# Optimization experiments

Measured on AMD Instinct MI355X. Metric: run time of the kernel, lower is better.

The kernel has to match this reference:

```python
import jax, jax.numpy as jnp
import numpy as np

NODE_TYPES = ["patient", "visit", "symptom", "procedure", "disease", "drug"]
N = {"patient": 20000, "visit": 100000, "symptom": 4000, "procedure": 8000,
     "disease": 10000, "drug": 4000}
D = 128          # embedding_dim == hidden_channels
N_LAYERS = 4     # conv1..conv4
# (src, dst) per relation; reverse edges included so every node type gets messages
REL = [("patient", "visit"), ("visit", "patient"),
       ("visit", "symptom"), ("symptom", "visit"),
       ("visit", "procedure"), ("procedure", "visit"),
       ("visit", "disease"), ("disease", "visit"),
       ("visit", "drug"), ("drug", "visit")]
E_FWD = {("patient", "visit"): 100000, ("visit", "symptom"): 300000,
         ("visit", "procedure"): 200000, ("visit", "disease"): 250000,
         ("visit", "drug"): 300000}
EI_NAMES = ["ei_pv", "ei_vp", "ei_vs", "ei_sv", "ei_vpr", "ei_prv",
            "ei_vd", "ei_dv", "ei_vdr", "ei_drv"]
E_LABEL = 200000


def setup_inputs() -> dict:
    key = jax.random.key(0)
    ks = iter(jax.random.split(key, 64))
    inp = {}
    for nt in NODE_TYPES:
        inp[f"node_id_{nt}"] = jnp.arange(N[nt], dtype=jnp.int32)
        inp[f"emb_{nt}"] = jax.random.normal(next(ks), (N[nt], D), jnp.float32)
    for name, (src, dst) in zip(EI_NAMES, REL):
        e = E_FWD.get((src, dst), E_FWD.get((dst, src)))
        row = jax.random.randint(next(ks), (e,), 0, N[src], dtype=jnp.int32)
        col = jax.random.randint(next(ks), (e,), 0, N[dst], dtype=jnp.int32)
        inp[name] = jnp.stack([row, col])
    R = len(REL)
    inp["W_l"] = jax.random.normal(next(ks), (N_LAYERS, R, D, D), jnp.float32) * 0.05
    inp["b_l"] = jnp.zeros((N_LAYERS, R, D), jnp.float32)
    inp["W_r"] = jax.random.normal(next(ks), (N_LAYERS, R, D, D), jnp.float32) * 0.05
    inp["cls_w1"] = jax.random.normal(next(ks), (2 * D, D), jnp.float32) * 0.05
    inp["cls_b1"] = jnp.zeros((D,), jnp.float32)
    inp["cls_w2"] = jax.random.normal(next(ks), (D, 1), jnp.float32) * 0.05
    inp["cls_b2"] = jnp.zeros((1,), jnp.float32)
    row = jax.random.randint(next(ks), (E_LABEL,), 0, N["visit"], dtype=jnp.int32)
    col = jax.random.randint(next(ks), (E_LABEL,), 0, N["drug"], dtype=jnp.int32)
    inp["edge_label_index"] = jnp.stack([row, col])
    inp["edge_label"] = jax.random.bernoulli(next(ks), 0.5, (E_LABEL,)).astype(jnp.float32)
    return inp


def _hetero_sage_layer(x, eis, Wl, bl, Wr):
    # to_hetero semantics: out[dst] = sum over edge types (src,rel,dst) of
    #   SAGEConv_rel: lin_l(mean_j x[src][j]) + lin_r(x[dst])   (PyG defaults)
    out = {nt: jnp.zeros_like(v) for nt, v in x.items()}
    for r, (src, dst) in enumerate(REL):
        ei = eis[r]
        n_dst = x[dst].shape[0]
        msg = jax.ops.segment_sum(x[src][ei[0]], ei[1], num_segments=n_dst)
        deg = jax.ops.segment_sum(jnp.ones((ei.shape[1],), x[src].dtype), ei[1],
                                  num_segments=n_dst)
        mean = msg / jnp.maximum(deg, 1.0)[:, None]  # empty segments stay 0 as in PyG
        out[dst] = out[dst] + mean @ Wl[r] + bl[r] + x[dst] @ Wr[r]
    return out


def reference(node_id_patient, node_id_visit, node_id_symptom, node_id_procedure,
              node_id_disease, node_id_drug,
              emb_patient, emb_visit, emb_symptom, emb_procedure, emb_disease, emb_drug,
              ei_pv, ei_vp, ei_vs, ei_sv, ei_vpr, ei_prv, ei_vd, ei_dv, ei_vdr, ei_drv,
              W_l, b_l, W_r, cls_w1, cls_b1, cls_w2, cls_b2,
              edge_label_index, edge_label):
    x = {"patient": emb_patient[node_id_patient],
         "visit": emb_visit[node_id_visit],
         "symptom": emb_symptom[node_id_symptom],
         "procedure": emb_procedure[node_id_procedure],
         "disease": emb_disease[node_id_disease],
         "drug": emb_drug[node_id_drug]}
    eis = [ei_pv, ei_vp, ei_vs, ei_sv, ei_vpr, ei_prv, ei_vd, ei_dv, ei_vdr, ei_drv]
    for l in range(N_LAYERS):
        x = _hetero_sage_layer(x, eis, W_l[l], b_l[l], W_r[l])
        if l < N_LAYERS - 1:  # relu after conv1..conv3 only; dropout is eval-mode identity
            x = {k: jax.nn.relu(v) for k, v in x.items()}
    # Classifier: gather visit/drug node features per labeled edge, concat, MLP
    zv = x["visit"][edge_label_index[0]]
    zd = x["drug"][edge_label_index[1]]
    h = jax.nn.relu(jnp.concatenate([zv, zd], axis=-1) @ cls_w1 + cls_b1)
    pred = (h @ cls_w2 + cls_b2).reshape(-1)
    # BCE with logits: softplus(z) - z*y, mean-reduced
    loss = jnp.mean(jax.nn.softplus(pred) - pred * edge_label)
    return loss, pred
```

## Files before the change

### kernel.cpp

```cpp
#include <hip/hip_runtime.h>
#include <cmath>


typedef _Float16 f16x8 __attribute__((ext_vector_type(8)));
typedef float f32x4 __attribute__((ext_vector_type(4)));

#define NREL 10
#define NCOUNTS 546000
#define NEDGES  2300000
#define NVISIT  100000
#define NVEDGES 1150000
#define PLW 546816
#define WT_ELEMS (4 * PLW + 69632)
#define XELEMS 18688000UL
#define SELEMS 5888000UL
#define NBKT 873
#define BCAP 5056
#define NMERGE 391
#define CONV_BLKS 9125

struct BkMeta {
  const int* ei[NREL]; int E[NREL]; int cbc[NREL]; int ndst[NREL];
  int sh[NREL]; int bb[NREL]; int nb[NREL];
};
struct PreMeta {
  const float* emb[6]; const int* nid[6]; int off[6];
  const float* W_l; const float* b_l; const float* W_r; const float* cw1;
  _Float16* Wt; float* visitSumB;
};
struct MTask {
  const _Float16* AH0; const _Float16* AL0;
  const _Float16* AH1; const _Float16* AL1;
  const _Float16* W;
  const float* bias;
  _Float16* outH; _Float16* outL;
  int M, blkOff, K, relu;
};
struct MMeta { MTask t[6]; int nTasks; };
struct F1Meta {
  const int* rp[5]; _Float16* mH[5]; _Float16* mL[5]; int aM[5]; int aOff[5];
  int nAgg; int aggTotal;
  const _Float16* gAH[5]; const _Float16* gAL[5]; const _Float16* gW[5];
  _Float16* gY[5]; int gM[5]; int gOff[5]; int nG;
};

__device__ __forceinline__ void conv0_body(const PreMeta& pm, int bc, int tid,
                                           _Float16* __restrict__ H,
                                           _Float16* __restrict__ L) {
  int i = bc * 256 + tid;
  if (i >= 146000 * 16) return;
  int g = i >> 4, q = i & 15;
  int t = 0;
  #pragma unroll
  for (int k = 1; k < 6; ++k) if (g >= pm.off[k]) t = k;
  int row = g - pm.off[t];
  int s = pm.nid[t][row];
  const float* p = pm.emb[t] + (size_t)s * 128 + q * 8;
  float4 v0 = *(const float4*)p;
  float4 v1 = *(const float4*)(p + 4);
  float v[8] = {v0.x, v0.y, v0.z, v0.w, v1.x, v1.y, v1.z, v1.w};
  f16x8 h, l;
  #pragma unroll
  for (int j = 0; j < 8; ++j) {
    h[j] = (_Float16)v[j];
    l[j] = (_Float16)(v[j] - (float)h[j]);
  }
  size_t o = (size_t)g * 128 + q * 8;
  *(f16x8*)(H + o) = h;
  *(f16x8*)(L + o) = l;
}

__device__ __forceinline__ void prep_body(const PreMeta& pm, int gid) {
  const int visitRel[5] = {0, 3, 5, 7, 9};
  const int inRel[5] = {1, 2, 4, 6, 8};
  if (gid < 1048576) {
    int l = gid >> 18, o = gid & 262143;
    float val; size_t wbase; int n, k, Kpad;
    if (o < 163840) {
      int t = o >> 15, e = o & 32767;
      k = e >> 7; n = e & 127; Kpad = 264;
      int r = inRel[t];
      val = (k < 128) ? pm.W_l[(size_t)(l * 10 + r) * 16384 + k * 128 + n]
                      : pm.W_r[(size_t)(l * 10 + r) * 16384 + (k - 128) * 128 + n];
      wbase = (size_t)l * PLW + t * 67584;
    } else if (o < 245760) {
      int q = (o - 163840) >> 14, e = (o - 163840) & 16383;
      k = e >> 7; n = e & 127; Kpad = 136;
      val = pm.W_l[(size_t)(l * 10 + visitRel[q]) * 16384 + k * 128 + n];
      wbase = (size_t)l * PLW + 337920 + q * 34816;
    } else {
      int e = o - 245760;
      k = e >> 7; n = e & 127; Kpad = 136;
      val = 0.f;
      #pragma unroll
      for (int q = 0; q < 5; ++q)
        val += pm.W_r[(size_t)(l * 10 + visitRel[q]) * 16384 + k * 128 + n];
      wbase = (size_t)l * PLW + 512000;
    }
    _Float16 h = (_Float16)val;
    _Float16 lo = (_Float16)(val - (float)h);
    pm.Wt[wbase + (size_t)n * Kpad + k] = h;
    pm.Wt[wbase + (size_t)(128 + n) * Kpad + k] = lo;
  } else if (gid < 1081344) {
    int e = gid - 1048576;
    int k = e >> 7, n = e & 127;
    float val = pm.cw1[(size_t)k * 128 + n];
    _Float16 h = (_Float16)val;
    _Float16 lo = (_Float16)(val - (float)h);
    size_t wbase = (size_t)4 * PLW + (k < 128 ? 0 : 34816);
    int kk = k & 127;
    pm.Wt[wbase + (size_t)n * 136 + kk] = h;
    pm.Wt[wbase + (size_t)(128 + n) * 136 + kk] = lo;
  } else if (gid < 1081856) {
    int e = gid - 1081344;
    int l = e >> 7, c = e & 127;
    float val = 0.f;
    #pragma unroll
    for (int q = 0; q < 5; ++q) val += pm.b_l[(l * 10 + visitRel[q]) * 128 + c];
    pm.visitSumB[e] = val;
  }
}

__global__ __launch_bounds__(256) void k1_p1_prep(BkMeta bm, PreMeta pm,
                                                  int* __restrict__ bcur,
                                                  int* __restrict__ bdata) {
  __shared__ int cnt[128];
  __shared__ int base[128];
  __shared__ unsigned short rnk[4096];
  int b = blockIdx.x;
  int tid = threadIdx.x;
  if (b >= 740) {
    prep_body(pm, (b - 740) * 256 + tid);
    return;
  }
  int r = b / 74;
  int bx = b - r * 74;
  int E = bm.E[r], sh = bm.sh[r], bb = bm.bb[r], nb = bm.nb[r];
  if (tid < 128) cnt[tid] = 0;
  __syncthreads();
  int e0 = bx * 4096;
  if (e0 >= E) return;
  const int* dstp = bm.ei[r] + E;
  const int* srcp = bm.ei[r];
  #pragma unroll
  for (int i = 0; i < 16; ++i) {
    int e = e0 + i * 256 + tid;
    if (e < E) {
      int bk = dstp[e] >> sh;
      rnk[i * 256 + tid] = (unsigned short)atomicAdd(&cnt[bk], 1);
    }
  }
  __syncthreads();
  if (tid < nb && cnt[tid] > 0) base[tid] = atomicAdd(&bcur[bb + tid], cnt[tid]);
  __syncthreads();
  #pragma unroll
  for (int i = 0; i < 16; ++i) {
    int e = e0 + i * 256 + tid;
    if (e < E) {
      int d = dstp[e];
      int bk = d >> sh;
      int pos = base[bk] + (int)rnk[i * 256 + tid];
      if (pos < BCAP)
        bdata[(size_t)(bb + bk) * BCAP + pos] = ((d & ((1 << sh) - 1)) << 17) | srcp[e];
    }
  }
}

__global__ __launch_bounds__(256) void k2_p2a_conv(BkMeta bm, PreMeta pm,
                                                   const int* __restrict__ bcur,
                                                   const int* __restrict__ bdata,
                                                   int* __restrict__ counts,
                                                   _Float16* __restrict__ H,
                                                   _Float16* __restrict__ L,
                                                   int convBase) {
  __shared__ int hist[2048];
  int b = blockIdx.x;
  int tid = threadIdx.x;
  if (b >= NBKT) {
    conv0_body(pm, convBase + b - NBKT, tid, H, L);
    return;
  }
  int g = b;
  int r = 0;
  #pragma unroll
  for (int i = 1; i < NREL; ++i) if (g >= bm.bb[i]) r = i;
  int lb = g - bm.bb[r];
  int sh = bm.sh[r], dpb = 1 << sh;
  for (int d = tid; d < dpb; d += 256) hist[d] = 0;
  __syncthreads();
  int cnt = bcur[g]; if (cnt > BCAP) cnt = BCAP;
  const int* bd = bdata + (size_t)g * BCAP;
  for (int i = tid; i < cnt; i += 256) atomicAdd(&hist[((unsigned)bd[i]) >> 17], 1);
  __syncthreads();
  int dBase = lb << sh;
  int dMax = bm.ndst[r] - dBase; if (dMax > dpb) dMax = dpb;
  for (int d = tid; d < dMax; d += 256) counts[bm.cbc[r] + dBase + d] = hist[d];
}

__global__ __launch_bounds__(1024) void scan1(const int* __restrict__ counts,
                                              int* __restrict__ partials) {
  __shared__ int s[1024];
  int i = blockIdx.x * 1024 + threadIdx.x;
  s[threadIdx.x] = (i < NCOUNTS) ? counts[i] : 0;
  __syncthreads();
  for (int off = 512; off > 0; off >>= 1) {
    if (threadIdx.x < off) s[threadIdx.x] += s[threadIdx.x + off];
    __syncthreads();
  }
  if (threadIdx.x == 0) partials[blockIdx.x] = s[0];
}

__global__ __launch_bounds__(1024) void scan2(int* __restrict__ partials, int nb) {
  __shared__ int s[1024];
  int t = threadIdx.x;
  int v = (t < nb) ? partials[t] : 0;
  s[t] = v;
  __syncthreads();
  for (int off = 1; off < 1024; off <<= 1) {
    int add = (t >= off) ? s[t - off] : 0;
    __syncthreads();
    s[t] += add;
    __syncthreads();
  }
  if (t < nb) partials[t] = s[t] - v;
}

__global__ __launch_bounds__(1024) void scan3(const int* __restrict__ counts,
                                              int* __restrict__ prefix,
                                              const int* __restrict__ partials) {
  __shared__ int s[1024];
  int t = threadIdx.x;
  int i = blockIdx.x * 1024 + t;
  int v = (i < NCOUNTS) ? counts[i] : 0;
  s[t] = v;
  __syncthreads();
  for (int off = 1; off < 1024; off <<= 1) {
    int add = (t >= off) ? s[t - off] : 0;
    __syncthreads();
    s[t] += add;
    __syncthreads();
  }
  int P = partials[blockIdx.x] + s[t] - v;
  if (i < NCOUNTS) prefix[i] = P;
  if (blockIdx.x == 0 && t == 0) prefix[NCOUNTS] = NEDGES;
}

__global__ __launch_bounds__(256) void k3_p2b_conv(BkMeta bm, PreMeta pm,
                                                   const int* __restrict__ bcur,
                                                   const int* __restrict__ bdata,
                                                   const int* __restrict__ prefix,
                                                   int* __restrict__ esrc,
                                                   _Float16* __restrict__ H,
                                                   _Float16* __restrict__ L,
                                                   int convBase) {
  __shared__ int pk[BCAP];
  __shared__ int srt[BCAP];
  __shared__ int cur[2048];
  __shared__ int part[256];
  __shared__ int baseSh;
  int b = blockIdx.x;
  int tid = threadIdx.x;
  if (b >= NBKT) {
    conv0_body(pm, convBase + b - NBKT, tid, H, L);
    return;
  }
  int g = b;
  int r = 0;
  #pragma unroll
  for (int i = 1; i < NREL; ++i) if (g >= bm.bb[i]) r = i;
  int lb = g - bm.bb[r];
  int sh = bm.sh[r], dpb = 1 << sh;
  int cnt = bcur[g]; if (cnt > BCAP) cnt = BCAP;
  const int* bd = bdata + (size_t)g * BCAP;
  for (int d = tid; d < dpb; d += 256) cur[d] = 0;
  for (int i = tid; i < cnt; i += 256) pk[i] = bd[i];
  __syncthreads();
  for (int i = tid; i < cnt; i += 256) atomicAdd(&cur[((unsigned)pk[i]) >> 17], 1);
  __syncthreads();
  int seg = (dpb + 255) >> 8;
  int s = 0;
  int b0 = tid * seg;
  for (int j = 0; j < seg; ++j) {
    int idx = b0 + j;
    if (idx < dpb) { int v = cur[idx]; cur[idx] = s; s += v; }
  }
  part[tid] = s;
  __syncthreads();
  for (int off = 1; off < 256; off <<= 1) {
    int add = (tid >= off) ? part[tid - off] : 0;
    __syncthreads();
    part[tid] += add;
    __syncthreads();
  }
  int myoff = part[tid] - s;
  for (int j = 0; j < seg; ++j) {
    int idx = b0 + j;
    if (idx < dpb) cur[idx] += myoff;
  }
  if (tid == 0) baseSh = prefix[bm.cbc[r] + (lb << sh)];
  __syncthreads();
  for (int i = tid; i < cnt; i += 256) {
    int p = pk[i];
    int pos = atomicAdd(&cur[((unsigned)p) >> 17], 1);
    srt[pos] = p & 0x1FFFF;
  }
  __syncthreads();
  int base = baseSh;
  for (int i = tid; i < cnt; i += 256) esrc[base + i] = srt[i];
}

__global__ __launch_bounds__(256) void k4_merge_conv(PreMeta pm,
                                                     const int* __restrict__ prefix,
                                                     const int* __restrict__ esrc,
                                                     int* __restrict__ mprefix,
                                                     int2* __restrict__ mesrc,
                                                     _Float16* __restrict__ H,
                                                     _Float16* __restrict__ L,
                                                     int convBase) {
  int b = blockIdx.x;
  int tid = threadIdx.x;
  if (b >= NMERGE) {
    conv0_body(pm, convBase + b - NMERGE, tid, H, L);
    return;
  }
  const int cbc[5]  = {0, 124000, 232000, 342000, 446000};
  const int yoff[5] = {0, 20000, 24000, 32000, 42000};
  int v = b * 256 + tid;
  if (v >= NVISIT) return;
  int e0[5], e1[5];
  int base = 0;
  #pragma unroll
  for (int q = 0; q < 5; ++q) {
    e0[q] = prefix[cbc[q] + v];
    e1[q] = prefix[cbc[q] + v + 1];
    base += e0[q] - prefix[cbc[q]];
  }
  mprefix[v] = base;
  if (v == NVISIT - 1) {
    int t = base;
    #pragma unroll
    for (int q = 0; q < 5; ++q) t += e1[q] - e0[q];
    mprefix[NVISIT] = t;
  }
  int pos = base;
  #pragma unroll
  for (int q = 0; q < 5; ++q) {
    int d = e1[q] - e0[q];
    if (d > 0) {
      int wb = __float_as_int(1.f / (float)d);
      for (int e = e0[q]; e < e1[q]; ++e)
        mesrc[pos++] = make_int2(yoff[q] + esrc[e], wb);
    }
  }
}

__global__ __launch_bounds__(256, 8) void fused1(F1Meta f,
                                                 const _Float16* __restrict__ xvH,
                                                 const int* __restrict__ esrc) {
  int b = blockIdx.x;
  int tid = threadIdx.x;
  if (b < f.aggTotal) {
    int t = 0;
    #pragma unroll
    for (int i = 1; i < 5; ++i) if (i < f.nAgg && b >= f.aOff[i]) t = i;
    int row = (b - f.aOff[t]) * 16 + (tid >> 4);
    if (row >= f.aM[t]) return;
    int q = tid & 15;
    const int* rp = f.rp[t];
    int e0 = rp[row], e1 = rp[row + 1];
    float a[8];
    #pragma unroll
    for (int j = 0; j < 8; ++j) a[j] = 0.f;
    int e = e0;
    for (; e + 4 <= e1; e += 4) {
      int s0 = esrc[e], s1 = esrc[e + 1], s2 = esrc[e + 2], s3 = esrc[e + 3];
      f16x8 v0 = *(const f16x8*)(xvH + (size_t)s0 * 128 + q * 8);
      f16x8 v1 = *(const f16x8*)(xvH + (size_t)s1 * 128 + q * 8);
      f16x8 v2 = *(const f16x8*)(xvH + (size_t)s2 * 128 + q * 8);
      f16x8 v3 = *(const f16x8*)(xvH + (size_t)s3 * 128 + q * 8);
      #pragma unroll
      for (int j = 0; j < 8; ++j)
        a[j] += ((float)v0[j] + (float)v1[j]) + ((float)v2[j] + (float)v3[j]);
    }
    for (; e < e1; ++e) {
      int s = esrc[e];
      f16x8 v = *(const f16x8*)(xvH + (size_t)s * 128 + q * 8);
      #pragma unroll
      for (int j = 0; j < 8; ++j) a[j] += (float)v[j];
    }
    float inv = (e1 > e0) ? 1.f / (float)(e1 - e0) : 0.f;
    f16x8 h, l;
    #pragma unroll
    for (int j = 0; j < 8; ++j) {
      float v = a[j] * inv;
      h[j] = (_Float16)v;
      l[j] = (_Float16)(v - (float)h[j]);
    }
    size_t o = (size_t)row * 128 + q * 8;
    *(f16x8*)(f.mH[t] + o) = h;
    *(f16x8*)(f.mL[t] + o) = l;
    return;
  }
  b -= f.aggTotal;
  int g = 0;
  #pragma unroll
  for (int i = 1; i < 5; ++i) if (i < f.nG && b >= f.gOff[i]) g = i;
  int blockRow = (b - f.gOff[g]) * 32;
  int lane = tid & 63, wave = tid >> 6;
  int quad = lane >> 4, lm = lane & 15;
  int wr = wave >> 1, wc = wave & 1;
  const _Float16* AH = f.gAH[g];
  const _Float16* AL = f.gAL[g];
  const _Float16* W = f.gW[g];
  int M = f.gM[g];
  int ar = blockRow + wr * 16 + lm;
  if (ar >= M) ar = M - 1;
  f32x4 acc[4];
  #pragma unroll
  for (int nt = 0; nt < 4; ++nt) acc[nt] = (f32x4){0.f, 0.f, 0.f, 0.f};
  for (int ks = 0; ks < 128; ks += 32) {
    f16x8 ah = *(const f16x8*)(AH + (size_t)ar * 128 + ks + quad * 8);
    f16x8 al = *(const f16x8*)(AL + (size_t)ar * 128 + ks + quad * 8);
    #pragma unroll
    for (int nt = 0; nt < 4; ++nt) {
      int n = wc * 64 + nt * 16 + lm;
      f16x8 bh = *(const f16x8*)(W + (size_t)n * 136 + ks + quad * 8);
      f16x8 bl = *(const f16x8*)(W + (size_t)(128 + n) * 136 + ks + quad * 8);
      acc[nt] = __builtin_amdgcn_mfma_f32_16x16x32_f16(ah, bh, acc[nt], 0, 0, 0);
      acc[nt] = __builtin_amdgcn_mfma_f32_16x16x32_f16(ah, bl, acc[nt], 0, 0, 0);
      acc[nt] = __builtin_amdgcn_mfma_f32_16x16x32_f16(al, bh, acc[nt], 0, 0, 0);
    }
  }
  _Float16* Y = f.gY[g];
  #pragma unroll
  for (int i = 0; i < 4; ++i) {
    int grow = blockRow + wr * 16 + quad * 4 + i;
    if (grow >= M) continue;
    #pragma unroll
    for (int nt = 0; nt < 4; ++nt)
      Y[(size_t)grow * 128 + wc * 64 + nt * 16 + lm] = (_Float16)acc[nt][i];
  }
}

__global__ __launch_bounds__(256) void agg_visit(const int* __restrict__ mprefix,
                                                 const int2* __restrict__ mesrc,
                                                 const _Float16* __restrict__ YH,
                                                 _Float16* __restrict__ xvH,
                                                 _Float16* __restrict__ xvL, int doRelu) {
  int row = blockIdx.x * 16 + (threadIdx.x >> 4);
  if (row >= NVISIT) return;
  int q = threadIdx.x & 15;
  size_t o = (size_t)row * 128 + q * 8;
  f16x8 h0 = *(f16x8*)(xvH + o);
  f16x8 l0 = *(f16x8*)(xvL + o);
  float a[8];
  #pragma unroll
  for (int j = 0; j < 8; ++j) a[j] = (float)h0[j] + (float)l0[j];
  int e0 = mprefix[row], e1 = mprefix[row + 1];
  int e = e0;
  for (; e + 4 <= e1; e += 4) {
    int2 p0 = mesrc[e], p1 = mesrc[e + 1], p2 = mesrc[e + 2], p3 = mesrc[e + 3];
    f16x8 v0 = *(const f16x8*)(YH + (size_t)p0.x * 128 + q * 8);
    f16x8 v1 = *(const f16x8*)(YH + (size_t)p1.x * 128 + q * 8);
    f16x8 v2 = *(const f16x8*)(YH + (size_t)p2.x * 128 + q * 8);
    f16x8 v3 = *(const f16x8*)(YH + (size_t)p3.x * 128 + q * 8);
    float w0 = __int_as_float(p0.y), w1 = __int_as_float(p1.y);
    float w2 = __int_as_float(p2.y), w3 = __int_as_float(p3.y);
    #pragma unroll
    for (int j = 0; j < 8; ++j)
      a[j] += (w0 * (float)v0[j] + w1 * (float)v1[j]) +
              (w2 * (float)v2[j] + w3 * (float)v3[j]);
  }
  for (; e < e1; ++e) {
    int2 p = mesrc[e];
    f16x8 v = *(const f16x8*)(YH + (size_t)p.x * 128 + q * 8);
    float w = __int_as_float(p.y);
    #pragma unroll
    for (int j = 0; j < 8; ++j) a[j] += w * (float)v[j];
  }
  f16x8 h, l;
  #pragma unroll
  for (int j = 0; j < 8; ++j) {
    float v = doRelu ? fmaxf(a[j], 0.f) : a[j];
    h[j] = (_Float16)v;
    l[j] = (_Float16)(v - (float)h[j]);
  }
  *(f16x8*)(xvH + o) = h;
  *(f16x8*)(xvL + o) = l;
}

__global__ __launch_bounds__(256, 2) void mgemm(MMeta mm) {
  int b = blockIdx.x;
  int ti = 0;
  for (int i = 1; i < mm.nTasks; ++i) if (b >= mm.t[i].blkOff) ti = i;
  MTask tk = mm.t[ti];
  int blockRow = (b - tk.blkOff) * 128;
  int Kpad = tk.K + 8;

  __shared__ _Float16 Ash[2][128][72];
  int tid = threadIdx.x;
  int wave = tid >> 6, lane = tid & 63;
  int quad = lane >> 4, lm = lane & 15;
  int wr = wave >> 1, wc = wave & 1;

  f32x4 acc[4][4];
  #pragma unroll
  for (int i = 0; i < 4; ++i)
    #pragma unroll
    for (int j = 0; j < 4; ++j) acc[i][j] = (f32x4){0.f, 0.f, 0.f, 0.f};

  const _Float16* wrowH[4];
  const _Float16* wrowL[4];
  #pragma unroll
  for (int nt = 0; nt < 4; ++nt) {
    int n = wc * 64 + nt * 16 + lm;
    wrowH[nt] = tk.W + (size_t)n * Kpad;
    wrowL[nt] = tk.W + (size_t)(128 + n) * Kpad;
  }

  int sr = tid >> 1, sk = (tid & 1) * 32;
  int gr = blockRow + sr; if (gr >= tk.M) gr = tk.M - 1;
  for (int k0 = 0; k0 < tk.K; k0 += 64) {
    const _Float16* AH = (k0 < 128) ? tk.AH0 : tk.AH1;
    const _Float16* AL = (k0 < 128) ? tk.AL0 : tk.AL1;
    size_t abase = (size_t)gr * 128 + (k0 & 127) + sk;
    #pragma unroll
    for (int c = 0; c < 4; ++c) {
      *(f16x8*)&Ash[0][sr][sk + c * 8] = *(const f16x8*)(AH + abase + c * 8);
      *(f16x8*)&Ash[1][sr][sk + c * 8] = *(const f16x8*)(AL + abase + c * 8);
    }
    __syncthreads();
    #pragma unroll
    for (int ks = 0; ks < 64; ks += 32) {
      int kf = k0 + ks + quad * 8;
      f16x8 bh[4], bl[4];
      #pragma unroll
      for (int nt = 0; nt < 4; ++nt) {
        bh[nt] = *(const f16x8*)(wrowH[nt] + kf);
        bl[nt] = *(const f16x8*)(wrowL[nt] + kf);
      }
      #pragma unroll
      for (int mt = 0; mt < 4; ++mt) {
        int r = wr * 64 + mt * 16 + lm;
        f16x8 ah = *(const f16x8*)&Ash[0][r][ks + quad * 8];
        f16x8 al = *(const f16x8*)&Ash[1][r][ks + quad * 8];
        #pragma unroll
        for (int nt = 0; nt < 4; ++nt) {
          acc[mt][nt] = __builtin_amdgcn_mfma_f32_16x16x32_f16(ah, bh[nt], acc[mt][nt], 0, 0, 0);
          acc[mt][nt] = __builtin_amdgcn_mfma_f32_16x16x32_f16(ah, bl[nt], acc[mt][nt], 0, 0, 0);
          acc[mt][nt] = __builtin_amdgcn_mfma_f32_16x16x32_f16(al, bh[nt], acc[mt][nt], 0, 0, 0);
        }
      }
    }
    __syncthreads();
  }

  float bv[4];
  #pragma unroll
  for (int nt = 0; nt < 4; ++nt)
    bv[nt] = tk.bias ? tk.bias[wc * 64 + nt * 16 + lm] : 0.f;
  #pragma unroll
  for (int mt = 0; mt < 4; ++mt) {
    #pragma unroll
    for (int i = 0; i < 4; ++i) {
      int grow = blockRow + wr * 64 + mt * 16 + quad * 4 + i;
      if (grow >= tk.M) continue;
      size_t ob = (size_t)grow * 128 + wc * 64 + lm;
      #pragma unroll
      for (int nt = 0; nt < 4; ++nt) {
        float v = acc[mt][nt][i] + bv[nt];
        if (tk.relu) v = fmaxf(v, 0.f);
        _Float16 h = (_Float16)v;
        tk.outH[ob + nt * 16] = h;
        if (tk.outL) tk.outL[ob + nt * 16] = (_Float16)(v - (float)h);
      }
    }
  }
}

__global__ __launch_bounds__(256) void cls_edge(
    const _Float16* __restrict__ UH, const _Float16* __restrict__ UL,
    const _Float16* __restrict__ VH, const _Float16* __restrict__ VL,
    const int* __restrict__ eli, const float* __restrict__ w2,
    const float* __restrict__ b2, const float* __restrict__ y,
    float* __restrict__ lossOut, float* __restrict__ pred, int M) {
  __shared__ float lsum[4];
  int tid = threadIdx.x;
  int q = tid & 15;
  int lane = tid & 63;
  float w2v[8];
  #pragma unroll
  for (int j = 0; j < 8; ++j) w2v[j] = w2[q * 8 + j];
  float bias = b2[0];
  float lacc = 0.f;
  int e0 = blockIdx.x * 128 + (tid >> 4);
  #pragma unroll
  for (int p = 0; p < 8; ++p) {
    int e = e0 + p * 16;
    if (e < M) {
      int vi = eli[e], di = eli[M + e];
      size_t uo = (size_t)vi * 128 + q * 8;
      size_t vo = (size_t)di * 128 + q * 8;
      f16x8 uh = *(const f16x8*)(UH + uo);
      f16x8 ul = *(const f16x8*)(UL + uo);
      f16x8 vh = *(const f16x8*)(VH + vo);
      f16x8 vl = *(const f16x8*)(VL + vo);
      float part = 0.f;
      #pragma unroll
      for (int j = 0; j < 8; ++j) {
        float t = ((float)uh[j] + (float)ul[j]) + ((float)vh[j] + (float)vl[j]);
        part += fmaxf(t, 0.f) * w2v[j];
      }
      part += __shfl_xor(part, 1);
      part += __shfl_xor(part, 2);
      part += __shfl_xor(part, 4);
      part += __shfl_xor(part, 8);
      if (q == 0) {
        float z = part + bias;
        pred[e] = z;
        lacc += fmaxf(z, 0.f) + log1pf(expf(-fabsf(z))) - z * y[e];
      }
    }
  }
  lacc += __shfl_xor(lacc, 16);
  lacc += __shfl_xor(lacc, 32);
  if (lane == 0) lsum[tid >> 6] = lacc;
  __syncthreads();
  if (tid == 0)
    atomicAdd(lossOut, (lsum[0] + lsum[1] + lsum[2] + lsum[3]) * (1.0f / 200000.0f));
}

extern "C" void kernel_launch(void* const* d_in, const int* in_sizes, int n_in,
                              void* d_out, int out_size, void* d_ws, size_t ws_size,
                              hipStream_t stream) {
  static const int kRows[6] = {20000, 100000, 4000, 8000, 10000, 4000};
  static const int kOff[6]  = {0, 20000, 120000, 124000, 132000, 142000};
  static const int kSmallT[5]   = {0, 2, 3, 4, 5};
  static const int kInRel[5]    = {1, 2, 4, 6, 8};
  static const int kCbcIn[5]    = {100000, 120000, 224000, 332000, 442000};
  static const int kYOff[5]     = {0, 20000, 24000, 32000, 42000};
  static const int kBOff[5]     = {0, 157, 189, 252, 331};
  static const int kAggOff[5]   = {0, 1250, 1500, 2000, 2625};
  static const int kLeanOff[5]  = {0, 625, 750, 1000, 1313};
  const int kAggTotal = 2875, kLeanTotal = 1438;
  const int kConvK2 = 3000, kConvK3 = 1500, kConvK4 = CONV_BLKS - 4500;
  static const int kCbcA[NREL]  = {0, 100000, 120000, 124000, 224000,
                                   232000, 332000, 342000, 442000, 446000};
  static const int kEhA[NREL]   = {100000, 100000, 300000, 300000, 200000,
                                   200000, 250000, 250000, 300000, 300000};
  static const int kNdst[NREL]  = {100000, 20000, 4000, 100000, 8000,
                                   100000, 10000, 100000, 4000, 100000};
  static const int kSh[NREL]    = {11, 9, 5, 10, 7, 10, 7, 10, 5, 10};
  static const int kNB[NREL]    = {49, 40, 125, 98, 63, 98, 79, 98, 125, 98};
  static const int kBB[NREL]    = {0, 49, 89, 214, 312, 375, 473, 552, 650, 775};

  const float* W_l = (const float*)d_in[22];
  const float* b_l = (const float*)d_in[23];
  const float* W_r = (const float*)d_in[24];
  const float* cw1 = (const float*)d_in[25];
  const float* cb1 = (const float*)d_in[26];
  const float* cw2 = (const float*)d_in[27];
  const float* cb2 = (const float*)d_in[28];
  const int* eli = (const int*)d_in[29];
  const float* ylab = (const float*)d_in[30];

  _Float16* H = (_Float16*)d_ws;
  _Float16* L = H + XELEMS;
  _Float16* meanH = L + XELEMS;
  _Float16* meanL = meanH + SELEMS;
  _Float16* YH = meanL + SELEMS;
  _Float16* Wt = YH + SELEMS;
  int* prefix = (int*)(Wt + WT_ELEMS);
  int* counts = prefix + 546004;
  int* esrc = counts + NCOUNTS;
  int* partials = esrc + NEDGES;
  float* visitSumB = (float*)(partials + 1024);
  int* bcur = (int*)(visitSumB + 512);
  int* bdata = bcur + 1024;

  int* mprefix = counts;
  int2* mesrc = (int2*)bdata;

  _Float16* UH = meanH;
  _Float16* VH = meanH + (size_t)NVISIT * 128;
  _Float16* VL = VH + (size_t)4000 * 128;
  _Float16* UL = (_Float16*)prefix;

  BkMeta bm;
  for (int r = 0; r < NREL; ++r) {
    bm.ei[r] = (const int*)d_in[12 + r];
    bm.E[r] = kEhA[r];
    bm.cbc[r] = kCbcA[r];
    bm.ndst[r] = kNdst[r];
    bm.sh[r] = kSh[r];
    bm.bb[r] = kBB[r];
    bm.nb[r] = kNB[r];
  }

  PreMeta pm;
  for (int t = 0; t < 6; ++t) {
    pm.nid[t] = (const int*)d_in[2 * t];
    pm.emb[t] = (const float*)d_in[2 * t + 1];
    pm.off[t] = kOff[t];
  }
  pm.W_l = W_l; pm.b_l = b_l; pm.W_r = W_r; pm.cw1 = cw1;
  pm.Wt = Wt; pm.visitSumB = visitSumB;

  hipMemsetAsync(bcur, 0, NBKT * sizeof(int), stream);
  hipMemsetAsync(d_out, 0, sizeof(float), stream);

  k1_p1_prep<<<dim3(740 + 4226), 256, 0, stream>>>(bm, pm, bcur, bdata);
  k2_p2a_conv<<<dim3(NBKT + kConvK2), 256, 0, stream>>>(bm, pm, bcur, bdata,
                                                        counts, H, L, 0);
  scan1<<<534, 1024, 0, stream>>>(counts, partials);
  scan2<<<1, 1024, 0, stream>>>(partials, 534);
  scan3<<<534, 1024, 0, stream>>>(counts, prefix, partials);
  k3_p2b_conv<<<dim3(NBKT + kConvK3), 256, 0, stream>>>(bm, pm, bcur, bdata,
                                                        prefix, esrc, H, L, kConvK2);
  k4_merge_conv<<<dim3(NMERGE + kConvK4), 256, 0, stream>>>(pm, prefix, esrc,
                                                            mprefix, mesrc, H, L,
                                                            kConvK2 + kConvK3);

  _Float16* xvH = H + (size_t)kOff[1] * 128;
  _Float16* xvL = L + (size_t)kOff[1] * 128;

  for (int l = 0; l < 4; ++l) {
    int doRelu = (l < 3);
    int last = (l == 3);
    _Float16* LW = Wt + (size_t)l * PLW;

    F1Meta f1;
    if (!last) {
      for (int t = 0; t < 5; ++t) {
        f1.rp[t] = prefix + kCbcIn[t];
        f1.mH[t] = meanH + (size_t)kYOff[t] * 128;
        f1.mL[t] = meanL + (size_t)kYOff[t] * 128;
        f1.aM[t] = kRows[kSmallT[t]];
        f1.aOff[t] = kAggOff[t];
      }
      f1.nAgg = 5;
      f1.aggTotal = kAggTotal;
    } else {
      f1.rp[0] = prefix + kCbcIn[4];
      f1.mH[0] = meanH + (size_t)kYOff[4] * 128;
      f1.mL[0] = meanL + (size_t)kYOff[4] * 128;
      f1.aM[0] = 4000;
      f1.aOff[0] = 0;
      for (int t = 1; t < 5; ++t) { f1.rp[t] = nullptr; f1.mH[t] = nullptr; f1.mL[t] = nullptr; f1.aM[t] = 0; f1.aOff[t] = 0; }
      f1.nAgg = 1;
      f1.aggTotal = 250;
    }
    for (int q = 0; q < 5; ++q) {
      size_t so = (size_t)kOff[kSmallT[q]] * 128;
      f1.gAH[q] = H + so;
      f1.gAL[q] = L + so;
      f1.gW[q] = LW + 337920 + (size_t)q * 34816;
      f1.gY[q] = YH + (size_t)kYOff[q] * 128;
      f1.gM[q] = kRows[kSmallT[q]];
      f1.gOff[q] = kLeanOff[q];
    }
    f1.nG = 5;
    fused1<<<dim3(f1.aggTotal + kLeanTotal), 256, 0, stream>>>(f1, xvH, esrc);

    MMeta m;
    if (!last) {
      m.nTasks = 6;
      for (int t = 0; t < 5; ++t) {
        size_t mo = (size_t)kYOff[t] * 128;
        size_t so = (size_t)kOff[kSmallT[t]] * 128;
        m.t[t].AH0 = meanH + mo; m.t[t].AL0 = meanL + mo;
        m.t[t].AH1 = H + so;     m.t[t].AL1 = L + so;
        m.t[t].W = LW + (size_t)t * 67584;
        m.t[t].bias = b_l + (size_t)(l * 10 + kInRel[t]) * 128;
        m.t[t].outH = H + so;    m.t[t].outL = L + so;
        m.t[t].M = kRows[kSmallT[t]];
        m.t[t].blkOff = kBOff[t];
        m.t[t].K = 256;
        m.t[t].relu = doRelu;
      }
      m.t[5].AH0 = xvH; m.t[5].AL0 = xvL;
      m.t[5].AH1 = nullptr; m.t[5].AL1 = nullptr;
      m.t[5].W = LW + 512000;
      m.t[5].bias = visitSumB + l * 128;
      m.t[5].outH = xvH; m.t[5].outL = xvL;
      m.t[5].M = NVISIT;
      m.t[5].blkOff = 363;
      m.t[5].K = 128;
      m.t[5].relu = 0;
      mgemm<<<dim3(363 + 782), 256, 0, stream>>>(m);
    } else {
      size_t mo = (size_t)kYOff[4] * 128;
      size_t so = (size_t)kOff[5] * 128;
      m.nTasks = 2;
      m.t[0].AH0 = meanH + mo; m.t[0].AL0 = meanL + mo;
      m.t[0].AH1 = H + so;     m.t[0].AL1 = L + so;
      m.t[0].W = LW + (size_t)4 * 67584;
      m.t[0].bias = b_l + (size_t)(l * 10 + kInRel[4]) * 128;
      m.t[0].outH = H + so;    m.t[0].outL = L + so;
      m.t[0].M = 4000;
      m.t[0].blkOff = 0;
      m.t[0].K = 256;
      m.t[0].relu = 0;
      m.t[1].AH0 = xvH; m.t[1].AL0 = xvL;
      m.t[1].AH1 = nullptr; m.t[1].AL1 = nullptr;
      m.t[1].W = LW + 512000;
      m.t[1].bias = visitSumB + l * 128;
      m.t[1].outH = xvH; m.t[1].outL = xvL;
      m.t[1].M = NVISIT;
      m.t[1].blkOff = 32;
      m.t[1].K = 128;
      m.t[1].relu = 0;
      mgemm<<<dim3(32 + 782), 256, 0, stream>>>(m);
    }

    agg_visit<<<dim3(6250), 256, 0, stream>>>(mprefix, mesrc, YH, xvH, xvL, doRelu);
  }

  MMeta muv;
  muv.nTasks = 2;
  muv.t[0].AH0 = xvH; muv.t[0].AL0 = xvL;
  muv.t[0].AH1 = nullptr; muv.t[0].AL1 = nullptr;
  muv.t[0].W = Wt + (size_t)4 * PLW;
  muv.t[0].bias = cb1;
  muv.t[0].outH = UH; muv.t[0].outL = UL;
  muv.t[0].M = NVISIT;
  muv.t[0].blkOff = 0;
  muv.t[0].K = 128;
  muv.t[0].relu = 0;
  muv.t[1].AH0 = H + (size_t)kOff[5] * 128; muv.t[1].AL0 = L + (size_t)kOff[5] * 128;
  muv.t[1].AH1 = nullptr; muv.t[1].AL1 = nullptr;
  muv.t[1].W = Wt + (size_t)4 * PLW + 34816;
  muv.t[1].bias = nullptr;
  muv.t[1].outH = VH; muv.t[1].outL = VL;
  muv.t[1].M = 4000;
  muv.t[1].blkOff = 782;
  muv.t[1].K = 128;
  muv.t[1].relu = 0;
  mgemm<<<dim3(782 + 32), 256, 0, stream>>>(muv);

  const int ML = 200000;
  cls_edge<<<dim3((ML + 127) / 128), 256, 0, stream>>>(
      UH, UL, VH, VL, eli, cw2, cb2, ylab,
      (float*)d_out, (float*)d_out + 1, ML);
}
```

Before: 905.2 us.

## Overlap conv0 prep work with scan kernels and shrink fused1 GEMM tiles

Spreads the conv0 conversion units across extra blocks appended to the three scan kernels and rebalances how many units each preprocessing kernel carries, so the small, latency-bound scans overlap with useful work. Separately, the lean GEMM part of fused1 now uses 16-row tiles with each wave owning 32 output columns, doubling the block count for more parallelism. The cost is extra parameters and branching in the scan kernels, scan blocks sharing the GPU with conv work, and more redundant weight loads per row in fused1.

```diff
diff --git a/kernel.cpp b/kernel.cpp
--- a/kernel.cpp
+++ b/kernel.cpp
@@ -198,7 +198,14 @@
 }
 
 __global__ __launch_bounds__(1024) void scan1(const int* __restrict__ counts,
-                                              int* __restrict__ partials) {
+                                              int* __restrict__ partials,
+                                              PreMeta pm, _Float16* __restrict__ H,
+                                              _Float16* __restrict__ L, int convBase) {
+  if (blockIdx.x >= 534) {
+    int unit = convBase + (blockIdx.x - 534) * 4 + (threadIdx.x >> 8);
+    conv0_body(pm, unit, threadIdx.x & 255, H, L);
+    return;
+  }
   __shared__ int s[1024];
   int i = blockIdx.x * 1024 + threadIdx.x;
   s[threadIdx.x] = (i < NCOUNTS) ? counts[i] : 0;
@@ -210,7 +217,14 @@
   if (threadIdx.x == 0) partials[blockIdx.x] = s[0];
 }
 
-__global__ __launch_bounds__(1024) void scan2(int* __restrict__ partials, int nb) {
+__global__ __launch_bounds__(1024) void scan2(int* __restrict__ partials, int nb,
+                                              PreMeta pm, _Float16* __restrict__ H,
+                                              _Float16* __restrict__ L, int convBase) {
+  if (blockIdx.x >= 1) {
+    int unit = convBase + (blockIdx.x - 1) * 4 + (threadIdx.x >> 8);
+    conv0_body(pm, unit, threadIdx.x & 255, H, L);
+    return;
+  }
   __shared__ int s[1024];
   int t = threadIdx.x;
   int v = (t < nb) ? partials[t] : 0;
@@ -227,7 +241,14 @@
 
 __global__ __launch_bounds__(1024) void scan3(const int* __restrict__ counts,
                                               int* __restrict__ prefix,
-                                              const int* __restrict__ partials) {
+                                              const int* __restrict__ partials,
+                                              PreMeta pm, _Float16* __restrict__ H,
+                                              _Float16* __restrict__ L, int convBase) {
+  if (blockIdx.x >= 534) {
+    int unit = convBase + (blockIdx.x - 534) * 4 + (threadIdx.x >> 8);
+    conv0_body(pm, unit, threadIdx.x & 255, H, L);
+    return;
+  }
   __shared__ int s[1024];
   int t = threadIdx.x;
   int i = blockIdx.x * 1024 + t;
@@ -405,25 +426,24 @@
   int g = 0;
   #pragma unroll
   for (int i = 1; i < 5; ++i) if (i < f.nG && b >= f.gOff[i]) g = i;
-  int blockRow = (b - f.gOff[g]) * 32;
+  int blockRow = (b - f.gOff[g]) * 16;
   int lane = tid & 63, wave = tid >> 6;
   int quad = lane >> 4, lm = lane & 15;
-  int wr = wave >> 1, wc = wave & 1;
   const _Float16* AH = f.gAH[g];
   const _Float16* AL = f.gAL[g];
   const _Float16* W = f.gW[g];
   int M = f.gM[g];
-  int ar = blockRow + wr * 16 + lm;
+  int ar = blockRow + lm;
   if (ar >= M) ar = M - 1;
-  f32x4 acc[4];
-  #pragma unroll
-  for (int nt = 0; nt < 4; ++nt) acc[nt] = (f32x4){0.f, 0.f, 0.f, 0.f};
+  f32x4 acc[2];
+  acc[0] = (f32x4){0.f, 0.f, 0.f, 0.f};
+  acc[1] = (f32x4){0.f, 0.f, 0.f, 0.f};
   for (int ks = 0; ks < 128; ks += 32) {
     f16x8 ah = *(const f16x8*)(AH + (size_t)ar * 128 + ks + quad * 8);
     f16x8 al = *(const f16x8*)(AL + (size_t)ar * 128 + ks + quad * 8);
     #pragma unroll
-    for (int nt = 0; nt < 4; ++nt) {
-      int n = wc * 64 + nt * 16 + lm;
+    for (int nt = 0; nt < 2; ++nt) {
+      int n = wave * 32 + nt * 16 + lm;
       f16x8 bh = *(const f16x8*)(W + (size_t)n * 136 + ks + quad * 8);
       f16x8 bl = *(const f16x8*)(W + (size_t)(128 + n) * 136 + ks + quad * 8);
       acc[nt] = __builtin_amdgcn_mfma_f32_16x16x32_f16(ah, bh, acc[nt], 0, 0, 0);
@@ -434,11 +454,11 @@
   _Float16* Y = f.gY[g];
   #pragma unroll
   for (int i = 0; i < 4; ++i) {
-    int grow = blockRow + wr * 16 + quad * 4 + i;
+    int grow = blockRow + quad * 4 + i;
     if (grow >= M) continue;
     #pragma unroll
-    for (int nt = 0; nt < 4; ++nt)
-      Y[(size_t)grow * 128 + wc * 64 + nt * 16 + lm] = (_Float16)acc[nt][i];
+    for (int nt = 0; nt < 2; ++nt)
+      Y[(size_t)grow * 128 + wave * 32 + nt * 16 + lm] = (_Float16)acc[nt][i];
   }
 }
 
@@ -641,9 +661,9 @@
   static const int kYOff[5]     = {0, 20000, 24000, 32000, 42000};
   static const int kBOff[5]     = {0, 157, 189, 252, 331};
   static const int kAggOff[5]   = {0, 1250, 1500, 2000, 2625};
-  static const int kLeanOff[5]  = {0, 625, 750, 1000, 1313};
-  const int kAggTotal = 2875, kLeanTotal = 1438;
-  const int kConvK2 = 3000, kConvK3 = 1500, kConvK4 = CONV_BLKS - 4500;
+  const int kAggTotal = 2875, kLeanTotal = 2875;
+  const int kConvK2 = 2000, kConvS1 = 500, kConvS2 = 375, kConvS3 = 500;
+  const int kConvK3 = 500, kConvK4 = 1125;
   static const int kCbcA[NREL]  = {0, 100000, 120000, 124000, 224000,
                                    232000, 332000, 342000, 442000, 446000};
   static const int kEhA[NREL]   = {100000, 100000, 300000, 300000, 200000,
@@ -712,14 +732,18 @@
   k1_p1_prep<<<dim3(740 + 4226), 256, 0, stream>>>(bm, pm, bcur, bdata);
   k2_p2a_conv<<<dim3(NBKT + kConvK2), 256, 0, stream>>>(bm, pm, bcur, bdata,
                                                         counts, H, L, 0);
-  scan1<<<534, 1024, 0, stream>>>(counts, partials);
-  scan2<<<1, 1024, 0, stream>>>(partials, 534);
-  scan3<<<534, 1024, 0, stream>>>(counts, prefix, partials);
+  int cb = kConvK2;
+  scan1<<<dim3(534 + kConvS1), 1024, 0, stream>>>(counts, partials, pm, H, L, cb);
+  cb += kConvS1 * 4;
+  scan2<<<dim3(1 + kConvS2), 1024, 0, stream>>>(partials, 534, pm, H, L, cb);
+  cb += kConvS2 * 4;
+  scan3<<<dim3(534 + kConvS3), 1024, 0, stream>>>(counts, prefix, partials, pm, H, L, cb);
+  cb += kConvS3 * 4;
   k3_p2b_conv<<<dim3(NBKT + kConvK3), 256, 0, stream>>>(bm, pm, bcur, bdata,
-                                                        prefix, esrc, H, L, kConvK2);
+                                                        prefix, esrc, H, L, cb);
+  cb += kConvK3;
   k4_merge_conv<<<dim3(NMERGE + kConvK4), 256, 0, stream>>>(pm, prefix, esrc,
-                                                            mprefix, mesrc, H, L,
-                                                            kConvK2 + kConvK3);
+                                                            mprefix, mesrc, H, L, cb);
 
   _Float16* xvH = H + (size_t)kOff[1] * 128;
   _Float16* xvL = L + (size_t)kOff[1] * 128;
@@ -757,7 +781,7 @@
       f1.gW[q] = LW + 337920 + (size_t)q * 34816;
       f1.gY[q] = YH + (size_t)kYOff[q] * 128;
       f1.gM[q] = kRows[kSmallT[q]];
-      f1.gOff[q] = kLeanOff[q];
+      f1.gOff[q] = kAggOff[q];
     }
     f1.nG = 5;
     fused1<<<dim3(f1.aggTotal + kLeanTotal), 256, 0, stream>>>(f1, xvH, esrc);
```

New measurement: 909.0 us. No clear change (+0.4%).
